# Performance work log

Measured on AMD Instinct MI355X. Metric: run time of the kernel, lower is better.

## Reference

```python
import jax, jax.numpy as jnp
import numpy as np
import math

B, L, D, H = 4, 1024, 1024, 16
HD = D // H

def setup_inputs() -> dict:
    rng = jax.random.key(0)
    ks = jax.random.split(rng, 11)
    def lin(k):
        # orthogonal-ish init not needed for numerics; normal scaled like torch default
        return jax.random.normal(k, (D, D), dtype=jnp.float32) * 0.02
    return {
        'key':   jax.random.normal(ks[0], (B, L, D), dtype=jnp.float32),
        'value': jax.random.normal(ks[1], (B, L, D), dtype=jnp.float32),
        'query': jax.random.normal(ks[2], (B, L, D), dtype=jnp.float32),
        'Wk': lin(ks[3]), 'bk': jnp.zeros((D,), jnp.float32),
        'Wq': lin(ks[4]), 'bq': jnp.zeros((D,), jnp.float32),
        'Wv': lin(ks[5]), 'bv': jnp.zeros((D,), jnp.float32),
        'Wp': lin(ks[6]), 'bp': jnp.zeros((D,), jnp.float32),
    }

def reference(key, value, query, Wk, bk, Wq, bq, Wv, bv, Wp, bp):
    # linear projections (torch Linear: x @ W.T + b)
    k = (key   @ Wk.T + bk).reshape(B, L, H, HD).transpose(0, 2, 1, 3)  # [B,H,L,hd]
    q = (query @ Wq.T + bq).reshape(B, L, H, HD).transpose(0, 2, 1, 3)
    v = (value @ Wv.T + bv).reshape(B, L, H, HD).transpose(0, 2, 1, 3)
    att = jnp.einsum('bhqd,bhkd->bhqk', q, k) * (1.0 / math.sqrt(HD))  # [B,H,L,L]
    causal = jnp.tril(jnp.ones((L, L), dtype=bool))
    att = jnp.where(causal[None, None], att, -jnp.inf)
    att = jax.nn.softmax(att, axis=-1)
    y = jnp.einsum('bhqk,bhkd->bhqd', att, v)  # [B,H,L,hd]
    y = y.transpose(0, 2, 1, 3).reshape(B, L, D)
    return y @ Wp.T + bp
```

## Files before the change

kernel.cpp:

```cpp
#include <hip/hip_runtime.h>

typedef unsigned short u16;
typedef __attribute__((ext_vector_type(8))) short bf16x8;
typedef __attribute__((ext_vector_type(4))) float f32x4;
typedef __attribute__((ext_vector_type(4))) unsigned short u16x4;

#define MFMA16 __builtin_amdgcn_mfma_f32_16x16x32_bf16

__device__ inline u16 f2bf(float f) {
    union { float f; unsigned u; } v; v.f = f;
    return (u16)((v.u + 0x8000u) >> 16);
}

__device__ inline void gld16(const u16* g, u16* l) {
    __builtin_amdgcn_global_load_lds(
        (const __attribute__((address_space(1))) unsigned int*)g,
        (__attribute__((address_space(3))) unsigned int*)l, 16, 0, 0);
}

struct CvtArgs { const float* src[7]; u16* dst[7]; };

__global__ __launch_bounds__(256) void cvt_kernel(CvtArgs a) {
    const int bid = blockIdx.x;
    int z, local;
    if (bid < 6144) { z = bid >> 11; local = bid & 2047; }
    else            { z = 3 + ((bid - 6144) >> 9); local = (bid - 6144) & 511; }
    const size_t i = ((size_t)local * 256 + threadIdx.x) * 8;
    const float* s = a.src[z];
    float4 v0 = *(const float4*)(s + i);
    float4 v1 = *(const float4*)(s + i + 4);
    union { u16 h[8]; bf16x8 v; } o;
    o.h[0] = f2bf(v0.x); o.h[1] = f2bf(v0.y); o.h[2] = f2bf(v0.z); o.h[3] = f2bf(v0.w);
    o.h[4] = f2bf(v1.x); o.h[5] = f2bf(v1.y); o.h[6] = f2bf(v1.z); o.h[7] = f2bf(v1.w);
    *(bf16x8*)(a.dst[z] + i) = o.v;
}

struct GemmArgs { const u16* A; const u16* W; const float* bias; void* out; int epi; };
struct Gemm3Args { GemmArgs g[3]; };

__global__ __launch_bounds__(256, 3) void gemm_qkv(Gemm3Args ga) {
    __shared__ u16 lA[128 * 64];
    __shared__ u16 lB[128 * 64];
    const GemmArgs g = ga.g[blockIdx.z];
    const int t = threadIdx.x, wave = t >> 6, lane = t & 63;
    const int quad = lane >> 4, l16 = lane & 15;
    const int bid = blockIdx.x;
    const int mtile = (bid & 7) * 4 + (bid >> 6);
    const int ntile = (bid >> 3) & 7;
    const int rowsA = mtile * 128, rowsB = ntile * 128;
    const int wm = (wave >> 1) * 64, wn = (wave & 1) * 64;
    const u16* A = g.A; const u16* W = g.W;

    f32x4 acc[4][4] = {};

    for (int kb = 0; kb < 1024; kb += 64) {
#pragma unroll
        for (int i = 0; i < 4; i++) {
            int u = (i * 4 + wave) * 64 + lane;
            int row = u >> 3, cu = (u & 7) ^ (row & 7);
            gld16(A + (size_t)(rowsA + row) * 1024 + kb + cu * 8, lA + u * 8);
        }
#pragma unroll
        for (int i = 0; i < 4; i++) {
            int u = (i * 4 + wave) * 64 + lane;
            int row = u >> 3, cu = (u & 7) ^ (row & 7);
            gld16(W + (size_t)(rowsB + row) * 1024 + kb + cu * 8, lB + u * 8);
        }
        __syncthreads();

        bf16x8 af[4][2], bfr[4][2];
#pragma unroll
        for (int mi = 0; mi < 4; mi++) {
            int row = wm + mi * 16 + l16;
#pragma unroll
            for (int kr = 0; kr < 2; kr++)
                af[mi][kr] = *(const bf16x8*)(lA + row * 64 + (((kr * 4 + quad) ^ (row & 7)) * 8));
        }
#pragma unroll
        for (int ni = 0; ni < 4; ni++) {
            int row = wn + ni * 16 + l16;
#pragma unroll
            for (int kr = 0; kr < 2; kr++)
                bfr[ni][kr] = *(const bf16x8*)(lB + row * 64 + (((kr * 4 + quad) ^ (row & 7)) * 8));
        }
#pragma unroll
        for (int mi = 0; mi < 4; mi++)
#pragma unroll
            for (int ni = 0; ni < 4; ni++) {
                acc[mi][ni] = MFMA16(af[mi][0], bfr[ni][0], acc[mi][ni], 0, 0, 0);
                acc[mi][ni] = MFMA16(af[mi][1], bfr[ni][1], acc[mi][ni], 0, 0, 0);
            }
        __syncthreads();
    }

    const int epi = g.epi;
#pragma unroll
    for (int ni = 0; ni < 4; ni++) {
        const int ncol = rowsB + wn + ni * 16 + l16;
        const float bv = g.bias[ncol];
        const int h = ncol >> 6, hd = ncol & 63;
#pragma unroll
        for (int mi = 0; mi < 4; mi++) {
            const int mrow0 = rowsA + wm + mi * 16 + quad * 4;
            const int b = mrow0 >> 10, l0 = mrow0 & 1023;
            if (epi == 0) {
#pragma unroll
                for (int r = 0; r < 4; r++)
                    ((u16*)g.out)[((size_t)(b * 16 + h) * 1024 + l0 + r) * 64 + hd] =
                        f2bf(acc[mi][ni][r] + bv);
            } else {
                u16x4 pk;
#pragma unroll
                for (int r = 0; r < 4; r++) pk[r] = f2bf(acc[mi][ni][r] + bv);
                *(u16x4*)((u16*)g.out + ((size_t)(b * 16 + h) * 64 + hd) * 1024 + l0) = pk;
            }
        }
    }
}

__global__ __launch_bounds__(256, 2) void gemm_p(const u16* __restrict__ A,
                                                 const u16* __restrict__ W,
                                                 const float* __restrict__ bias,
                                                 float* __restrict__ out)
{
    __shared__ u16 lA[128 * 64];
    __shared__ u16 lB[64 * 64];
    const int t = threadIdx.x, wave = t >> 6, lane = t & 63;
    const int quad = lane >> 4, l16 = lane & 15;
    const int bid = blockIdx.x;
    const int mtile = (bid & 7) * 4 + (bid >> 7);
    const int ntile = (bid >> 3) & 15;
    const int rowsA = mtile * 128, rowsB = ntile * 64;
    const int wm = (wave >> 1) * 64, wn = (wave & 1) * 32;

    f32x4 acc[4][2] = {};

    for (int kb = 0; kb < 1024; kb += 64) {
#pragma unroll
        for (int i = 0; i < 4; i++) {
            int u = (i * 4 + wave) * 64 + lane;
            int row = u >> 3, cu = (u & 7) ^ (row & 7);
            gld16(A + (size_t)(rowsA + row) * 1024 + kb + cu * 8, lA + u * 8);
        }
#pragma unroll
        for (int i = 0; i < 2; i++) {
            int u = (i * 4 + wave) * 64 + lane;
            int row = u >> 3, cu = (u & 7) ^ (row & 7);
            gld16(W + (size_t)(rowsB + row) * 1024 + kb + cu * 8, lB + u * 8);
        }
        __syncthreads();

        bf16x8 af[4][2], bfr[2][2];
#pragma unroll
        for (int mi = 0; mi < 4; mi++) {
            int row = wm + mi * 16 + l16;
#pragma unroll
            for (int kr = 0; kr < 2; kr++)
                af[mi][kr] = *(const bf16x8*)(lA + row * 64 + (((kr * 4 + quad) ^ (row & 7)) * 8));
        }
#pragma unroll
        for (int ni = 0; ni < 2; ni++) {
            int row = wn + ni * 16 + l16;
#pragma unroll
            for (int kr = 0; kr < 2; kr++)
                bfr[ni][kr] = *(const bf16x8*)(lB + row * 64 + (((kr * 4 + quad) ^ (row & 7)) * 8));
        }
#pragma unroll
        for (int mi = 0; mi < 4; mi++)
#pragma unroll
            for (int ni = 0; ni < 2; ni++) {
                acc[mi][ni] = MFMA16(af[mi][0], bfr[ni][0], acc[mi][ni], 0, 0, 0);
                acc[mi][ni] = MFMA16(af[mi][1], bfr[ni][1], acc[mi][ni], 0, 0, 0);
            }
        __syncthreads();
    }

#pragma unroll
    for (int ni = 0; ni < 2; ni++) {
        const int ncol = rowsB + wn + ni * 16 + l16;
        const float bv = bias[ncol];
#pragma unroll
        for (int mi = 0; mi < 4; mi++) {
            const int mrow0 = rowsA + wm + mi * 16 + quad * 4;
#pragma unroll
            for (int r = 0; r < 4; r++)
                out[(size_t)(mrow0 + r) * 1024 + ncol] = acc[mi][ni][r] + bv;
        }
    }
}

__global__ __launch_bounds__(256, 4) void attn_kernel(const u16* __restrict__ qh,
                                                      const u16* __restrict__ kh,
                                                      const u16* __restrict__ vhT,
                                                      u16* __restrict__ y)
{
    __shared__ u16 sK[64 * 64];
    __shared__ u16 sVT[64 * 64];
    __shared__ u16 sP[4 * 16 * 72];

    const int t = threadIdx.x, wave = t >> 6, lane = t & 63;
    const int quad = lane >> 4, l16 = lane & 15;
    const int x = blockIdx.x, bh = blockIdx.y;
    const int qb = (x < 8) ? x : 23 - x;
    const int qbase = qb * 64 + wave * 16;
    const size_t base = (size_t)bh * 1024 * 64;
    const float e2 = 0.18033688f;

    bf16x8 aq[2];
#pragma unroll
    for (int kr = 0; kr < 2; kr++)
        aq[kr] = *(const bf16x8*)(qh + base + (size_t)(qbase + l16) * 64 + kr * 32 + quad * 8);

    bf16x8 ones;
#pragma unroll
    for (int j = 0; j < 8; j++) ones[j] = (short)0x3F80;

    f32x4 o[4] = {};
    f32x4 lacc = {};
    u16* pw = sP + wave * 16 * 72;

    const int nkb = qb + 1;
    for (int kb = 0; kb < nkb; kb++) {
        const int krow0 = kb * 64;
#pragma unroll
        for (int i = 0; i < 2; i++) {
            int u = (i * 4 + wave) * 64 + lane;
            int row = u >> 3, cu = (u & 7) ^ (row & 7);
            gld16(kh + base + (size_t)(krow0 + row) * 64 + cu * 8, sK + u * 8);
        }
#pragma unroll
        for (int i = 0; i < 2; i++) {
            int u = (i * 4 + wave) * 64 + lane;
            int row = u >> 3, cu = (u & 7) ^ (row & 7);
            gld16(vhT + ((size_t)(bh * 64 + row)) * 1024 + krow0 + cu * 8, sVT + u * 8);
        }
        __syncthreads();

        bf16x8 bk[4][2];
#pragma unroll
        for (int kc = 0; kc < 4; kc++) {
            int row = kc * 16 + l16;
#pragma unroll
            for (int kr = 0; kr < 2; kr++)
                bk[kc][kr] = *(const bf16x8*)(sK + row * 64 + (((kr * 4 + quad) ^ (row & 7)) * 8));
        }
        f32x4 sc[4];
        __builtin_amdgcn_s_setprio(1);
#pragma unroll
        for (int kc = 0; kc < 4; kc++) {
            f32x4 z = {};
            z = MFMA16(aq[0], bk[kc][0], z, 0, 0, 0);
            z = MFMA16(aq[1], bk[kc][1], z, 0, 0, 0);
            sc[kc] = z;
        }
        __builtin_amdgcn_s_setprio(0);
        const bool dm = (krow0 + 63 > qbase);
#pragma unroll
        for (int kc = 0; kc < 4; kc++)
#pragma unroll
            for (int r = 0; r < 4; r++) {
                float xv = fminf(sc[kc][r] * e2, 43.f);
                float pv = exp2f(xv);
                if (dm) {
                    int kcol = krow0 + kc * 16 + l16;
                    int qrow = qbase + quad * 4 + r;
                    if (kcol > qrow) pv = 0.f;
                }
                pw[(quad * 4 + r) * 72 + kc * 16 + l16] = f2bf(pv);
            }
        bf16x8 bv[4][2];
#pragma unroll
        for (int nt = 0; nt < 4; nt++) {
            int row = nt * 16 + l16;
#pragma unroll
            for (int kr = 0; kr < 2; kr++)
                bv[nt][kr] = *(const bf16x8*)(sVT + row * 64 + (((kr * 4 + quad) ^ (row & 7)) * 8));
        }
        bf16x8 ap0 = *(const bf16x8*)(pw + l16 * 72 + quad * 8);
        bf16x8 ap1 = *(const bf16x8*)(pw + l16 * 72 + 32 + quad * 8);
        __builtin_amdgcn_s_setprio(1);
#pragma unroll
        for (int nt = 0; nt < 4; nt++) {
            o[nt] = MFMA16(ap0, bv[nt][0], o[nt], 0, 0, 0);
            o[nt] = MFMA16(ap1, bv[nt][1], o[nt], 0, 0, 0);
        }
        lacc = MFMA16(ap0, ones, lacc, 0, 0, 0);
        lacc = MFMA16(ap1, ones, lacc, 0, 0, 0);
        __builtin_amdgcn_s_setprio(0);
        __syncthreads();
    }

    const int b = bh >> 4, h = bh & 15;
#pragma unroll
    for (int nt = 0; nt < 4; nt++)
#pragma unroll
        for (int r = 0; r < 4; r++) {
            int qrow = qbase + quad * 4 + r;
            int d = nt * 16 + l16;
            y[(size_t)(b * 1024 + qrow) * 1024 + h * 64 + d] = f2bf(o[nt][r] / lacc[r]);
        }
}

extern "C" void kernel_launch(void* const* d_in, const int* in_sizes, int n_in,
                              void* d_out, int out_size, void* d_ws, size_t ws_size,
                              hipStream_t stream)
{
    const float* key   = (const float*)d_in[0];
    const float* value = (const float*)d_in[1];
    const float* query = (const float*)d_in[2];
    const float* Wk = (const float*)d_in[3];
    const float* bk = (const float*)d_in[4];
    const float* Wq = (const float*)d_in[5];
    const float* bq = (const float*)d_in[6];
    const float* Wv = (const float*)d_in[7];
    const float* bv = (const float*)d_in[8];
    const float* Wp = (const float*)d_in[9];
    const float* bp = (const float*)d_in[10];

    char* ws = (char*)d_ws;
    u16* xq  = (u16*)(ws + (size_t)( 0 << 20));
    u16* xk  = (u16*)(ws + (size_t)( 8 << 20));
    u16* xv  = (u16*)(ws + (size_t)(16 << 20));
    u16* wqb = (u16*)(ws + (size_t)(24 << 20));
    u16* wkb = (u16*)(ws + (size_t)(26 << 20));
    u16* wvb = (u16*)(ws + (size_t)(28 << 20));
    u16* wpb = (u16*)(ws + (size_t)(30 << 20));
    u16* qh  = (u16*)(ws + (size_t)(32 << 20));
    u16* kh  = (u16*)(ws + (size_t)(40 << 20));
    u16* vhT = (u16*)(ws + (size_t)(48 << 20));
    u16* y   = xq;

    CvtArgs ca;
    ca.src[0] = query; ca.dst[0] = xq;
    ca.src[1] = key;   ca.dst[1] = xk;
    ca.src[2] = value; ca.dst[2] = xv;
    ca.src[3] = Wq;    ca.dst[3] = wqb;
    ca.src[4] = Wk;    ca.dst[4] = wkb;
    ca.src[5] = Wv;    ca.dst[5] = wvb;
    ca.src[6] = Wp;    ca.dst[6] = wpb;
    hipLaunchKernelGGL(cvt_kernel, dim3(8192), dim3(256), 0, stream, ca);

    Gemm3Args g3;
    g3.g[0] = GemmArgs{xq, wqb, bq, (void*)qh,  0};
    g3.g[1] = GemmArgs{xk, wkb, bk, (void*)kh,  0};
    g3.g[2] = GemmArgs{xv, wvb, bv, (void*)vhT, 2};
    hipLaunchKernelGGL(gemm_qkv, dim3(256, 1, 3), dim3(256), 0, stream, g3);

    hipLaunchKernelGGL(attn_kernel, dim3(16, 64), dim3(256), 0, stream, qh, kh, vhT, y);

    hipLaunchKernelGGL(gemm_p, dim3(512), dim3(256), 0, stream, y, wpb, bp, (float*)d_out);
}
```

Measured before the change: 210.0 us.

## Pair causal query blocks per workgroup and double-buffer K/V tiles in attention

Each attention workgroup now handles two query blocks (pr and 15-pr), so every block does the same total work and each loaded K/V tile serves both query tiles. K and V^T tiles are double-buffered in LDS, with the next tile's async loads issued before the current tile is computed. The grid becomes 512 blocks with a remapped bh index, and launch bounds drop to 2 waves-per-EU occupancy to allow the extra registers. The cost is more register pressure and fewer resident blocks, plus serialized use of the shared P scratch for the two tiles.

```diff
diff --git a/kernel.cpp b/kernel.cpp
--- a/kernel.cpp
+++ b/kernel.cpp
@@ -189,52 +189,67 @@
     }
 }
 
-__global__ __launch_bounds__(256, 4) void attn_kernel(const u16* __restrict__ qh,
+__global__ __launch_bounds__(256, 2) void attn_kernel(const u16* __restrict__ qh,
                                                       const u16* __restrict__ kh,
                                                       const u16* __restrict__ vhT,
                                                       u16* __restrict__ y)
 {
-    __shared__ u16 sK[64 * 64];
-    __shared__ u16 sVT[64 * 64];
+    __shared__ u16 sK[2][64 * 64];
+    __shared__ u16 sVT[2][64 * 64];
     __shared__ u16 sP[4 * 16 * 72];
 
     const int t = threadIdx.x, wave = t >> 6, lane = t & 63;
     const int quad = lane >> 4, l16 = lane & 15;
-    const int x = blockIdx.x, bh = blockIdx.y;
-    const int qb = (x < 8) ? x : 23 - x;
-    const int qbase = qb * 64 + wave * 16;
+    const int bid = blockIdx.x;
+    const int bh = (bid & 7) * 8 + ((bid >> 3) & 7);
+    const int pr = bid >> 6;
+    const int qbaseA = pr * 64 + wave * 16;
+    const int qbaseB = (15 - pr) * 64 + wave * 16;
     const size_t base = (size_t)bh * 1024 * 64;
     const float e2 = 0.18033688f;
 
-    bf16x8 aq[2];
-#pragma unroll
-    for (int kr = 0; kr < 2; kr++)
-        aq[kr] = *(const bf16x8*)(qh + base + (size_t)(qbase + l16) * 64 + kr * 32 + quad * 8);
+    bf16x8 aqA[2], aqB[2];
+#pragma unroll
+    for (int kr = 0; kr < 2; kr++) {
+        aqA[kr] = *(const bf16x8*)(qh + base + (size_t)(qbaseA + l16) * 64 + kr * 32 + quad * 8);
+        aqB[kr] = *(const bf16x8*)(qh + base + (size_t)(qbaseB + l16) * 64 + kr * 32 + quad * 8);
+    }
 
     bf16x8 ones;
 #pragma unroll
     for (int j = 0; j < 8; j++) ones[j] = (short)0x3F80;
 
-    f32x4 o[4] = {};
-    f32x4 lacc = {};
+    f32x4 oA[4] = {}, oB[4] = {};
+    f32x4 laccA = {}, laccB = {};
     u16* pw = sP + wave * 16 * 72;
 
-    const int nkb = qb + 1;
-    for (int kb = 0; kb < nkb; kb++) {
+    auto STAGE = [&](int kb, int b) {
         const int krow0 = kb * 64;
 #pragma unroll
         for (int i = 0; i < 2; i++) {
             int u = (i * 4 + wave) * 64 + lane;
             int row = u >> 3, cu = (u & 7) ^ (row & 7);
-            gld16(kh + base + (size_t)(krow0 + row) * 64 + cu * 8, sK + u * 8);
+            gld16(kh + base + (size_t)(krow0 + row) * 64 + cu * 8, &sK[b][0] + u * 8);
         }
 #pragma unroll
         for (int i = 0; i < 2; i++) {
             int u = (i * 4 + wave) * 64 + lane;
             int row = u >> 3, cu = (u & 7) ^ (row & 7);
-            gld16(vhT + ((size_t)(bh * 64 + row)) * 1024 + krow0 + cu * 8, sVT + u * 8);
-        }
-        __syncthreads();
+            gld16(vhT + ((size_t)(bh * 64 + row)) * 1024 + krow0 + cu * 8, &sVT[b][0] + u * 8);
+        }
+    };
+
+    STAGE(0, 0);
+    __syncthreads();
+
+    const int last = 15 - pr;
+    int cur = 0;
+    for (int kb = 0; kb <= last; kb++) {
+        if (kb < last) STAGE(kb + 1, cur ^ 1);
+        const int krow0 = kb * 64;
+        const bool actA = (kb <= pr);
+        const u16* sKc = sK[cur];
+        const u16* sVc = sVT[cur];
 
         bf16x8 bk[4][2];
 #pragma unroll
@@ -242,52 +257,94 @@
             int row = kc * 16 + l16;
 #pragma unroll
             for (int kr = 0; kr < 2; kr++)
-                bk[kc][kr] = *(const bf16x8*)(sK + row * 64 + (((kr * 4 + quad) ^ (row & 7)) * 8));
-        }
-        f32x4 sc[4];
+                bk[kc][kr] = *(const bf16x8*)(sKc + row * 64 + (((kr * 4 + quad) ^ (row & 7)) * 8));
+        }
+        f32x4 scA[4], scB[4];
         __builtin_amdgcn_s_setprio(1);
 #pragma unroll
         for (int kc = 0; kc < 4; kc++) {
             f32x4 z = {};
-            z = MFMA16(aq[0], bk[kc][0], z, 0, 0, 0);
-            z = MFMA16(aq[1], bk[kc][1], z, 0, 0, 0);
-            sc[kc] = z;
+            z = MFMA16(aqB[0], bk[kc][0], z, 0, 0, 0);
+            z = MFMA16(aqB[1], bk[kc][1], z, 0, 0, 0);
+            scB[kc] = z;
+        }
+        if (actA) {
+#pragma unroll
+            for (int kc = 0; kc < 4; kc++) {
+                f32x4 z = {};
+                z = MFMA16(aqA[0], bk[kc][0], z, 0, 0, 0);
+                z = MFMA16(aqA[1], bk[kc][1], z, 0, 0, 0);
+                scA[kc] = z;
+            }
         }
         __builtin_amdgcn_s_setprio(0);
-        const bool dm = (krow0 + 63 > qbase);
-#pragma unroll
-        for (int kc = 0; kc < 4; kc++)
-#pragma unroll
-            for (int r = 0; r < 4; r++) {
-                float xv = fminf(sc[kc][r] * e2, 43.f);
-                float pv = exp2f(xv);
-                if (dm) {
-                    int kcol = krow0 + kc * 16 + l16;
-                    int qrow = qbase + quad * 4 + r;
-                    if (kcol > qrow) pv = 0.f;
+
+        bf16x8 apA0, apA1, apB0, apB1;
+        if (actA) {
+            const bool dmA = (krow0 + 63 > qbaseA);
+#pragma unroll
+            for (int kc = 0; kc < 4; kc++)
+#pragma unroll
+                for (int r = 0; r < 4; r++) {
+                    float xv = fminf(scA[kc][r] * e2, 43.f);
+                    float pv = exp2f(xv);
+                    if (dmA) {
+                        int kcol = krow0 + kc * 16 + l16;
+                        int qrow = qbaseA + quad * 4 + r;
+                        if (kcol > qrow) pv = 0.f;
+                    }
+                    pw[(quad * 4 + r) * 72 + kc * 16 + l16] = f2bf(pv);
                 }
-                pw[(quad * 4 + r) * 72 + kc * 16 + l16] = f2bf(pv);
-            }
+            apA0 = *(const bf16x8*)(pw + l16 * 72 + quad * 8);
+            apA1 = *(const bf16x8*)(pw + l16 * 72 + 32 + quad * 8);
+        }
+        {
+            const bool dmB = (krow0 + 63 > qbaseB);
+#pragma unroll
+            for (int kc = 0; kc < 4; kc++)
+#pragma unroll
+                for (int r = 0; r < 4; r++) {
+                    float xv = fminf(scB[kc][r] * e2, 43.f);
+                    float pv = exp2f(xv);
+                    if (dmB) {
+                        int kcol = krow0 + kc * 16 + l16;
+                        int qrow = qbaseB + quad * 4 + r;
+                        if (kcol > qrow) pv = 0.f;
+                    }
+                    pw[(quad * 4 + r) * 72 + kc * 16 + l16] = f2bf(pv);
+                }
+            apB0 = *(const bf16x8*)(pw + l16 * 72 + quad * 8);
+            apB1 = *(const bf16x8*)(pw + l16 * 72 + 32 + quad * 8);
+        }
+
         bf16x8 bv[4][2];
 #pragma unroll
         for (int nt = 0; nt < 4; nt++) {
             int row = nt * 16 + l16;
 #pragma unroll
             for (int kr = 0; kr < 2; kr++)
-                bv[nt][kr] = *(const bf16x8*)(sVT + row * 64 + (((kr * 4 + quad) ^ (row & 7)) * 8));
-        }
-        bf16x8 ap0 = *(const bf16x8*)(pw + l16 * 72 + quad * 8);
-        bf16x8 ap1 = *(const bf16x8*)(pw + l16 * 72 + 32 + quad * 8);
+                bv[nt][kr] = *(const bf16x8*)(sVc + row * 64 + (((kr * 4 + quad) ^ (row & 7)) * 8));
+        }
         __builtin_amdgcn_s_setprio(1);
 #pragma unroll
         for (int nt = 0; nt < 4; nt++) {
-            o[nt] = MFMA16(ap0, bv[nt][0], o[nt], 0, 0, 0);
-            o[nt] = MFMA16(ap1, bv[nt][1], o[nt], 0, 0, 0);
-        }
-        lacc = MFMA16(ap0, ones, lacc, 0, 0, 0);
-        lacc = MFMA16(ap1, ones, lacc, 0, 0, 0);
+            oB[nt] = MFMA16(apB0, bv[nt][0], oB[nt], 0, 0, 0);
+            oB[nt] = MFMA16(apB1, bv[nt][1], oB[nt], 0, 0, 0);
+        }
+        laccB = MFMA16(apB0, ones, laccB, 0, 0, 0);
+        laccB = MFMA16(apB1, ones, laccB, 0, 0, 0);
+        if (actA) {
+#pragma unroll
+            for (int nt = 0; nt < 4; nt++) {
+                oA[nt] = MFMA16(apA0, bv[nt][0], oA[nt], 0, 0, 0);
+                oA[nt] = MFMA16(apA1, bv[nt][1], oA[nt], 0, 0, 0);
+            }
+            laccA = MFMA16(apA0, ones, laccA, 0, 0, 0);
+            laccA = MFMA16(apA1, ones, laccA, 0, 0, 0);
+        }
         __builtin_amdgcn_s_setprio(0);
         __syncthreads();
+        cur ^= 1;
     }
 
     const int b = bh >> 4, h = bh & 15;
@@ -295,9 +352,11 @@
     for (int nt = 0; nt < 4; nt++)
 #pragma unroll
         for (int r = 0; r < 4; r++) {
-            int qrow = qbase + quad * 4 + r;
             int d = nt * 16 + l16;
-            y[(size_t)(b * 1024 + qrow) * 1024 + h * 64 + d] = f2bf(o[nt][r] / lacc[r]);
+            int qrA = qbaseA + quad * 4 + r;
+            int qrB = qbaseB + quad * 4 + r;
+            y[(size_t)(b * 1024 + qrA) * 1024 + h * 64 + d] = f2bf(oA[nt][r] / laccA[r]);
+            y[(size_t)(b * 1024 + qrB) * 1024 + h * 64 + d] = f2bf(oB[nt][r] / laccB[r]);
         }
 }
 
@@ -346,7 +405,7 @@
     g3.g[2] = GemmArgs{xv, wvb, bv, (void*)vhT, 2};
     hipLaunchKernelGGL(gemm_qkv, dim3(256, 1, 3), dim3(256), 0, stream, g3);
 
-    hipLaunchKernelGGL(attn_kernel, dim3(16, 64), dim3(256), 0, stream, qh, kh, vhT, y);
+    hipLaunchKernelGGL(attn_kernel, dim3(512), dim3(256), 0, stream, qh, kh, vhT, y);
 
     hipLaunchKernelGGL(gemm_p, dim3(512), dim3(256), 0, stream, y, wpb, bp, (float*)d_out);
 }
```

New measurement: 191.4 us. 8.9% less time.
